# Kernel tuning notes

Measured on AMD Instinct MI355X. Metric: run time of the kernel, lower is better.

The kernel has to match this reference:

```python
import jax, jax.numpy as jnp
import numpy as np

B, N_VIS, N_TXT = 2, 2048, 256
N_HEAD, HEAD_DIM = 16, 64
C = N_HEAD * HEAD_DIM  # 1024
EPS = 1e-6


def setup_inputs() -> dict:
    key = jax.random.key(0)
    ks = jax.random.split(key, 24)
    s = 0.02
    inp = {
        'vis_x': jax.random.normal(ks[0], (B, N_VIS, C), jnp.float32),
        'txt_x': jax.random.normal(ks[1], (B, N_TXT, C), jnp.float32),
        'rope_cos': jax.random.uniform(ks[2], (N_VIS, HEAD_DIM), jnp.float32, -1.0, 1.0),
        'rope_sin': jax.random.uniform(ks[3], (N_VIS, HEAD_DIM), jnp.float32, -1.0, 1.0),
    }
    names = ['vis_qw', 'vis_kw', 'vis_vw', 'vis_ow', 'txt_qw', 'txt_kw', 'txt_vw', 'txt_ow']
    for i, n in enumerate(names):
        inp[n] = jax.random.normal(ks[4 + i], (C, C), jnp.float32) * s
        inp[n[:-1] + 'b'] = jnp.zeros((C,), jnp.float32)
    for n in ['vis_qn', 'vis_kn', 'txt_qn', 'txt_kn']:
        inp[n] = jnp.ones((HEAD_DIM,), jnp.float32)
    return inp


def _heads(x, w, b):
    # x: [B,N,C] -> [B,H,N,D]  (torch Linear: x @ W.T + b)
    y = x @ w.T + b
    Bn, N, _ = y.shape
    return y.reshape(Bn, N, N_HEAD, HEAD_DIM).transpose(0, 2, 1, 3)


def _rmsnorm(x, g):
    return x * jax.lax.rsqrt(jnp.mean(x * x, axis=-1, keepdims=True) + EPS) * g


def _rope(x, cos, sin):
    # interleaved-pair rotation: pairs (x0,x1) -> (-x1, x0)
    xr, xi = x[..., 0::2], x[..., 1::2]
    rot = jnp.stack([-xi, xr], axis=-1).reshape(x.shape)
    return x * cos[None, None] + rot * sin[None, None]


def reference(vis_x, txt_x, rope_cos, rope_sin,
              vis_qw, vis_qb, vis_kw, vis_kb, vis_vw, vis_vb, vis_ow, vis_ob,
              txt_qw, txt_qb, txt_kw, txt_kb, txt_vw, txt_vb, txt_ow, txt_ob,
              vis_qn, vis_kn, txt_qn, txt_kn):
    q_vis = _rmsnorm(_heads(vis_x, vis_qw, vis_qb), vis_qn)
    k_vis = _rmsnorm(_heads(vis_x, vis_kw, vis_kb), vis_kn)
    v_vis = _heads(vis_x, vis_vw, vis_vb)
    q_txt = _rmsnorm(_heads(txt_x, txt_qw, txt_qb), txt_qn)
    k_txt = _rmsnorm(_heads(txt_x, txt_kw, txt_kb), txt_kn)
    v_txt = _heads(txt_x, txt_vw, txt_vb)

    q_vis = _rope(q_vis, rope_cos, rope_sin)
    k_vis = _rope(k_vis, rope_cos, rope_sin)

    q = jnp.concatenate([q_txt, q_vis], axis=2)  # [B,H,S,D]
    k = jnp.concatenate([k_txt, k_vis], axis=2)
    v = jnp.concatenate([v_txt, v_vis], axis=2)

    scale = 1.0 / jnp.sqrt(jnp.asarray(HEAD_DIM, q.dtype))
    scores = jnp.einsum('bhqd,bhkd->bhqk', q, k) * scale
    attn = jax.nn.softmax(scores, axis=-1)
    out = jnp.einsum('bhqk,bhkd->bhqd', attn, v)  # [B,H,S,D]

    txt_out = out[:, :, :N_TXT, :].transpose(0, 2, 1, 3).reshape(q.shape[0], N_TXT, C)
    vis_out = out[:, :, N_TXT:, :].transpose(0, 2, 1, 3).reshape(q.shape[0], N_VIS, C)
    vis_out = vis_out @ vis_ow.T + vis_ob
    txt_out = txt_out @ txt_ow.T + txt_ob
    return (vis_out, txt_out)
```

## Files before the change

### kernel.cpp

```cpp
#include <hip/hip_runtime.h>

typedef _Float16 h8 __attribute__((ext_vector_type(8)));
typedef _Float16 h4 __attribute__((ext_vector_type(4)));
typedef _Float16 h2 __attribute__((ext_vector_type(2)));
typedef float f4 __attribute__((ext_vector_type(4)));
typedef float f16x16 __attribute__((ext_vector_type(16)));

#define LOG2E 1.44269504088896340736f

#define BARRIER_ACQ do { __builtin_amdgcn_s_barrier(); \
                         asm volatile("" ::: "memory"); } while (0)
#define BARRIER_REL do { asm volatile("" ::: "memory"); \
                         __builtin_amdgcn_s_barrier(); } while (0)

__device__ __forceinline__ void gload_lds16(const void* g, void* l) {
    __builtin_amdgcn_global_load_lds(
        (const __attribute__((address_space(1))) void*)g,
        (__attribute__((address_space(3))) void*)l, 16, 0, 0);
}

struct CastArgs { const float* src[10]; _Float16* dst[10]; };

__global__ __launch_bounds__(256) void cast_all_kernel(CastArgs a) {
    int blk = blockIdx.x;
    int seg, rel;
    if (blk < 4096)      { seg = 0; rel = blk; }
    else if (blk < 4608) { seg = 1; rel = blk - 4096; }
    else { int t = blk - 4608; seg = 2 + (t >> 10); rel = t & 1023; }
    long base = ((long)rel * 256 + threadIdx.x) * 4;
    float4 v = *(const float4*)(a.src[seg] + base);
    h4 o = { (_Float16)v.x, (_Float16)v.y, (_Float16)v.z, (_Float16)v.w };
    *(h4*)(a.dst[seg] + base) = o;
}

struct GemmDesc {
    const _Float16* A[2];
    const _Float16* W[2];
    char*           C[2];
    const float*    bias[2][3];
    long bsA[2];
    long aoff[2];
    long bsC[2];
    int  mshift[2];
    int  mcut;
};

template<bool OUT_F32>
__global__ __launch_bounds__(256)
void gemm_kernel(GemmDesc g, int K, int N, int gm, int gn, int xgn)
{
    __shared__ __align__(16) _Float16 As[2][128 * 64];
    __shared__ __align__(16) _Float16 Bs[2][128 * 64];
    const int lane = threadIdx.x & 63;
    const int wave = threadIdx.x >> 6;
    const int lid = blockIdx.x;
    const int xcd = lid & 7;
    const int r0 = lid >> 3;
    const int mtile = (xcd / xgn) * gm + (r0 % gm);
    const int ntile = (xcd % xgn) * gn + (r0 / gm);

    const int seg = mtile >= g.mcut;
    const int mloc = mtile - (seg ? g.mcut : 0);
    const int bidx = mloc >> g.mshift[seg];
    const int min_ = mloc & ((1 << g.mshift[seg]) - 1);
    const _Float16* Ab = g.A[seg] + (long)bidx * g.bsA[seg] + g.aoff[seg]
                         + (long)min_ * 128 * K;
    const _Float16* Bb = g.W[seg] + (long)ntile * 128 * K;
    const long crow0 = (long)bidx * g.bsC[seg] + (long)min_ * 128 * N;

    const int wr = wave >> 1, wc = wave & 1;
    f4 acc[4][4] = {};

    auto stage = [&](int bf, int kt) {
#pragma unroll
        for (int it = 0; it < 4; ++it) {
            int r = wave * 32 + it * 8 + (lane >> 3);
            int lc = (lane & 7) ^ (r & 7);
            gload_lds16((const char*)(Ab + (long)r * K + kt) + lc * 16,
                        (char*)&As[bf][0] + (wave * 32 + it * 8) * 128);
            gload_lds16((const char*)(Bb + (long)r * K + kt) + lc * 16,
                        (char*)&Bs[bf][0] + (wave * 32 + it * 8) * 128);
        }
    };

    const int nk = K >> 6;
    stage(0, 0);
    int buf = 0;
#pragma unroll 1
    for (int ki = 0; ki < nk; ++ki) {
        if (ki + 1 < nk) {
            stage(buf ^ 1, (ki + 1) << 6);
            asm volatile("s_waitcnt vmcnt(8)" ::: "memory");
        } else {
            asm volatile("s_waitcnt vmcnt(0)" ::: "memory");
        }
        BARRIER_ACQ;
#pragma unroll
        for (int kk = 0; kk < 2; ++kk) {
            h8 af[4], bf4[4];
#pragma unroll
            for (int m = 0; m < 4; ++m) {
                int row = wr * 64 + m * 16 + (lane & 15);
                int pc = (kk * 4 + (lane >> 4)) ^ (row & 7);
                af[m] = *(const h8*)(&As[buf][row * 64 + pc * 8]);
            }
#pragma unroll
            for (int n = 0; n < 4; ++n) {
                int row = wc * 64 + n * 16 + (lane & 15);
                int pc = (kk * 4 + (lane >> 4)) ^ (row & 7);
                bf4[n] = *(const h8*)(&Bs[buf][row * 64 + pc * 8]);
            }
#pragma unroll
            for (int m = 0; m < 4; ++m)
#pragma unroll
                for (int n = 0; n < 4; ++n)
                    acc[m][n] = __builtin_amdgcn_mfma_f32_16x16x32_f16(
                        af[m], bf4[n], acc[m][n], 0, 0, 0);
        }
        BARRIER_REL;
        buf ^= 1;
    }

#pragma unroll
    for (int n = 0; n < 4; ++n) {
        int col = ntile * 128 + wc * 64 + n * 16 + (lane & 15);
        const float* bp = (col < 1024) ? g.bias[seg][0]
                        : (col < 2048) ? g.bias[seg][1] : g.bias[seg][2];
        float bv = bp[col & 1023];
#pragma unroll
        for (int m = 0; m < 4; ++m) {
            int lrow = wr * 64 + m * 16 + ((lane >> 4) << 2);
#pragma unroll
            for (int r = 0; r < 4; ++r) {
                float v = acc[m][n][r] + bv;
                long off = crow0 + (long)(lrow + r) * N + col;
                if (OUT_F32) ((float*)g.C[seg])[off] = v;
                else         ((_Float16*)g.C[seg])[off] = (_Float16)v;
            }
        }
    }
}

__device__ __forceinline__ float ssum8(h8 v) {
    float s = 0.f;
#pragma unroll
    for (int j = 0; j < 8; ++j) { float f = (float)v[j]; s += f * f; }
    return s;
}
__device__ __forceinline__ float red8(float s) {
    s += __shfl_xor(s, 1); s += __shfl_xor(s, 2); s += __shfl_xor(s, 4);
    return s;
}
__device__ __forceinline__ h8 norm_rope(h8 v, float rs_, const float* g, float gmul,
                                        const float* cs, const float* sn, int vis) {
    float f[8];
#pragma unroll
    for (int j = 0; j < 8; ++j) f[j] = (float)v[j] * rs_ * g[j] * gmul;
    h8 o;
    if (vis) {
#pragma unroll
        for (int j = 0; j < 8; j += 2) {
            float a = f[j], b = f[j + 1];
            o[j]     = (_Float16)(a * cs[j]     - b * sn[j]);
            o[j + 1] = (_Float16)(b * cs[j + 1] + a * sn[j + 1]);
        }
    } else {
#pragma unroll
        for (int j = 0; j < 8; ++j) o[j] = (_Float16)f[j];
    }
    return o;
}

__global__ __launch_bounds__(256)
void pass2_kernel(const _Float16* __restrict__ Yv, const _Float16* __restrict__ Yt,
                  const float* __restrict__ gqv, const float* __restrict__ gkv_,
                  const float* __restrict__ gqt, const float* __restrict__ gkt,
                  const float* __restrict__ rc, const float* __restrict__ rs,
                  _Float16* __restrict__ Q, _Float16* __restrict__ Kd,
                  _Float16* __restrict__ Vt)
{
    const int wave = threadIdx.x >> 6;
    const int lane = threadIdx.x & 63;
    const int row = blockIdx.x * 4 + wave;
    const int is_vis = row < 4096;
    const _Float16* y;
    const float *gq, *gk;
    int b, n, npos;
    if (is_vis) {
        y = Yv + (long)row * 3072; gq = gqv; gk = gkv_;
        b = row >> 11; n = row & 2047; npos = 256 + n;
    } else {
        int r2 = row - 4096;
        y = Yt + (long)r2 * 3072; gq = gqt; gk = gkt;
        b = r2 >> 8; n = r2 & 255; npos = n;
    }
    const int h0 = lane >> 3;
    const int d0 = (lane & 7) * 8;

    h8 q0 = *(const h8*)(y + lane * 8);
    h8 q1 = *(const h8*)(y + 512 + lane * 8);
    h8 k0 = *(const h8*)(y + 1024 + lane * 8);
    h8 k1 = *(const h8*)(y + 1536 + lane * 8);
    h8 v0 = *(const h8*)(y + 2048 + lane * 8);
    h8 v1 = *(const h8*)(y + 2560 + lane * 8);

    float ga[8], gb[8];
    *(float4*)(ga)     = *(const float4*)(gq + d0);
    *(float4*)(ga + 4) = *(const float4*)(gq + d0 + 4);
    *(float4*)(gb)     = *(const float4*)(gk + d0);
    *(float4*)(gb + 4) = *(const float4*)(gk + d0 + 4);
    float cs[8], sn[8];
    if (is_vis) {
        *(float4*)(cs)     = *(const float4*)(rc + n * 64 + d0);
        *(float4*)(cs + 4) = *(const float4*)(rc + n * 64 + d0 + 4);
        *(float4*)(sn)     = *(const float4*)(rs + n * 64 + d0);
        *(float4*)(sn + 4) = *(const float4*)(rs + n * 64 + d0 + 4);
    }

    const float rq0 = rsqrtf(red8(ssum8(q0)) * (1.0f / 64.0f) + 1e-6f);
    const float rq1 = rsqrtf(red8(ssum8(q1)) * (1.0f / 64.0f) + 1e-6f);
    const float rk0 = rsqrtf(red8(ssum8(k0)) * (1.0f / 64.0f) + 1e-6f);
    const float rk1 = rsqrtf(red8(ssum8(k1)) * (1.0f / 64.0f) + 1e-6f);

    const float qmul = 0.125f * LOG2E;
    const long obA = (((long)b * 16 + h0)      * 2304 + npos) * 64 + d0;
    const long obB = (((long)b * 16 + h0 + 8)  * 2304 + npos) * 64 + d0;
    *(h8*)(Q + obA)  = norm_rope(q0, rq0, ga, qmul, cs, sn, is_vis);
    *(h8*)(Q + obB)  = norm_rope(q1, rq1, ga, qmul, cs, sn, is_vis);
    *(h8*)(Kd + obA) = norm_rope(k0, rk0, gb, 1.0f, cs, sn, is_vis);
    *(h8*)(Kd + obB) = norm_rope(k1, rk1, gb, 1.0f, cs, sn, is_vis);

    const long vbA = ((long)(b * 16 + h0)     * 64 + d0) * 2304 + npos;
    const long vbB = ((long)(b * 16 + h0 + 8) * 64 + d0) * 2304 + npos;
#pragma unroll
    for (int j = 0; j < 8; ++j) {
        Vt[vbA + (long)j * 2304] = v0[j];
        Vt[vbB + (long)j * 2304] = v1[j];
    }
}

__device__ __forceinline__ void attn_stage(const char* Kt, const char* Vt, char* S,
                                           int bufB, int t,
                                           int gK0, int gK1, int gV0, int gV1,
                                           int ldsW) {
    const char* kt = Kt + (long)t * 8192;
    const char* vt = Vt + (long)t * 128;
    gload_lds16(kt + gK0, S + bufB + ldsW);
    gload_lds16(kt + gK1, S + bufB + 4096 + ldsW);
    gload_lds16(vt + gV0, S + 16384 + bufB + ldsW);
    gload_lds16(vt + gV1, S + 16384 + bufB + 4096 + ldsW);
}

__device__ __forceinline__ void pv_half(const float* p, const char* S, int vbase,
                                        const int* off, int kblk,
                                        f16x16* oacc, float& psum) {
    const h2 one2 = {(_Float16)1.f, (_Float16)1.f};
#pragma unroll
    for (int kb = 0; kb < 2; ++kb) {
        unsigned w0 = __builtin_bit_cast(unsigned,
            __builtin_amdgcn_cvt_pkrtz(p[8 * kb + 0], p[8 * kb + 1]));
        unsigned w1 = __builtin_bit_cast(unsigned,
            __builtin_amdgcn_cvt_pkrtz(p[8 * kb + 2], p[8 * kb + 3]));
        unsigned w2 = __builtin_bit_cast(unsigned,
            __builtin_amdgcn_cvt_pkrtz(p[8 * kb + 4], p[8 * kb + 5]));
        unsigned w3 = __builtin_bit_cast(unsigned,
            __builtin_amdgcn_cvt_pkrtz(p[8 * kb + 6], p[8 * kb + 7]));
        psum = __builtin_amdgcn_fdot2(__builtin_bit_cast(h2, w0), one2, psum, false);
        psum = __builtin_amdgcn_fdot2(__builtin_bit_cast(h2, w1), one2, psum, false);
        psum = __builtin_amdgcn_fdot2(__builtin_bit_cast(h2, w2), one2, psum, false);
        psum = __builtin_amdgcn_fdot2(__builtin_bit_cast(h2, w3), one2, psum, false);
        asm("v_permlane32_swap_b32 %0, %1" : "+v"(w0), "+v"(w2));
        asm("v_permlane32_swap_b32 %0, %1" : "+v"(w1), "+v"(w3));
        union { unsigned u[4]; h8 v; } pa;
        pa.u[0] = w0; pa.u[1] = w1; pa.u[2] = w2; pa.u[3] = w3;
#pragma unroll
        for (int dblk = 0; dblk < 2; ++dblk) {
            h8 vb = *(const h8*)(S + vbase + dblk * 4096 + off[kblk * 2 + kb]);
            oacc[dblk] = __builtin_amdgcn_mfma_f32_32x32x16_f16(
                pa.v, vb, oacc[dblk], 0, 0, 0);
        }
    }
}

__device__ __forceinline__ void attn_tile(const char* S, int bufB, const int* off,
                                          const h8* qf, f16x16* oacc, float& psum) {
    const f16x16 kZero = {};
    f16x16 st0, st1;
    {
        h8 ka0 = *(const h8*)(S + bufB + off[0]);
        h8 ka1 = *(const h8*)(S + bufB + 4096 + off[0]);
        st0 = __builtin_amdgcn_mfma_f32_32x32x16_f16(ka0, qf[0], kZero, 0, 0, 0);
        st1 = __builtin_amdgcn_mfma_f32_32x32x16_f16(ka1, qf[0], kZero, 0, 0, 0);
    }
#pragma unroll
    for (int ds = 1; ds < 4; ++ds) {
        h8 ka0 = *(const h8*)(S + bufB + off[ds]);
        h8 ka1 = *(const h8*)(S + bufB + 4096 + off[ds]);
        st0 = __builtin_amdgcn_mfma_f32_32x32x16_f16(ka0, qf[ds], st0, 0, 0, 0);
        st1 = __builtin_amdgcn_mfma_f32_32x32x16_f16(ka1, qf[ds], st1, 0, 0, 0);
    }
    float p0[16], p1[16];
#pragma unroll
    for (int r = 0; r < 16; ++r) { p0[r] = exp2f(st0[r]); p1[r] = exp2f(st1[r]); }
    pv_half(p0, S, 16384 + bufB, off, 0, oacc, psum);
    pv_half(p1, S, 16384 + bufB, off, 1, oacc, psum);
}

__global__ __launch_bounds__(256, 4)
void attn_kernel(const _Float16* __restrict__ Qg,
                 const _Float16* __restrict__ Kg,
                 const _Float16* __restrict__ Vg,
                 _Float16* __restrict__ Op,
                 float* __restrict__ Lp,
                 int nt, int cpx)
{
    __shared__ __align__(16) char S[32768];
    const int lane = threadIdx.x & 63;
    const int wave = threadIdx.x >> 6;
    const int l31 = lane & 31, hi = lane >> 5;
    const int d0 = blockIdx.x;
    const int id = (d0 & 7) * cpx + (d0 >> 3);
    const int split = id / 576;
    const int rem = id - split * 576;
    const int bh = rem / 18;
    const int qb = rem - bh * 18;
    const int b = bh >> 4, h = bh & 15;
    const _Float16* Qbh = Qg + (long)bh * 2304 * 64;
    const char* Kt = (const char*)(Kg + (long)bh * 2304 * 64) + (long)split * nt * 8192;
    const char* Vt = (const char*)(Vg + (long)bh * 64 * 2304) + (long)split * nt * 128;
    _Float16* Ops = Op + (long)split * 4718592;
    float* Lps = Lp + (long)split * 73728;
    const int q0 = qb * 128 + wave * 32;

    h8 qf[4];
#pragma unroll
    for (int ds = 0; ds < 4; ++ds)
        qf[ds] = *(const h8*)(Qbh + (long)(q0 + l31) * 64 + ds * 16 + hi * 8);

    const int sg16 = ((lane & 7) ^ (lane >> 3)) * 16;
    const int rK = wave * 8 + (lane >> 3);
    const int gK0 = rK * 128 + sg16;
    const int gK1 = gK0 + 32 * 128;
    const int gV0 = rK * 4608 + sg16;
    const int gV1 = gV0 + 32 * 4608;
    const int ldsW = wave * 1024;
    int off[4];
#pragma unroll
    for (int j = 0; j < 4; ++j)
        off[j] = l31 * 128 + (((j * 2 + hi) ^ (l31 & 7)) * 16);

    f16x16 oacc[2] = {};
    float psum = 0.f;

    attn_stage(Kt, Vt, S, 0, 0, gK0, gK1, gV0, gV1, ldsW);
    int buf = 0;
#pragma unroll 1
    for (int t = 0; t < nt; ++t) {
        if (t + 1 < nt) {
            attn_stage(Kt, Vt, S, (buf ^ 1) * 8192, t + 1, gK0, gK1, gV0, gV1, ldsW);
            asm volatile("s_waitcnt vmcnt(4)" ::: "memory");
        } else {
            asm volatile("s_waitcnt vmcnt(0)" ::: "memory");
        }
        BARRIER_ACQ;
        __builtin_amdgcn_s_setprio(1);
        attn_tile(S, buf * 8192, off, qf, oacc, psum);
        __builtin_amdgcn_s_setprio(0);
        BARRIER_REL;
        buf ^= 1;
    }

    float lsum = psum + __shfl_xor(psum, 32);
    if (hi == 0) Lps[(long)bh * 2304 + q0 + l31] = lsum;
#pragma unroll
    for (int dblk = 0; dblk < 2; ++dblk) {
        int dcol = h * 64 + dblk * 32 + l31;
#pragma unroll
        for (int r = 0; r < 16; ++r) {
            int qrow = q0 + (r & 3) + 8 * (r >> 2) + 4 * hi;
            Ops[((long)b * 2304 + qrow) * 1024 + dcol] = (_Float16)oacc[dblk][r];
        }
    }
}

__global__ __launch_bounds__(256)
void combine_kernel(const _Float16* __restrict__ Op,
                    const float* __restrict__ Lp,
                    _Float16* __restrict__ Oh, int ns)
{
    long i = ((long)blockIdx.x * 256 + threadIdx.x) * 8;
    long row = i >> 10;
    int bb = row >= 2304;
    int n = (int)row - bb * 2304;
    int h = ((int)i & 1023) >> 6;
    long lidx = ((long)(bb * 16 + h)) * 2304 + n;
    float l = 0.f;
    float acc[8] = {};
    for (int s = 0; s < ns; ++s) {
        l += Lp[(long)s * 73728 + lidx];
        h8 a = *(const h8*)(Op + (long)s * 4718592 + i);
#pragma unroll
        for (int j = 0; j < 8; ++j) acc[j] += (float)a[j];
    }
    float inv = 1.0f / l;
    h8 o;
#pragma unroll
    for (int j = 0; j < 8; ++j) o[j] = (_Float16)(acc[j] * inv);
    *(h8*)(Oh + i) = o;
}

extern "C" void kernel_launch(void* const* d_in, const int* in_sizes, int n_in,
                              void* d_out, int out_size, void* d_ws, size_t ws_size,
                              hipStream_t stream)
{
    const float* vis_x    = (const float*)d_in[0];
    const float* txt_x    = (const float*)d_in[1];
    const float* rope_cos = (const float*)d_in[2];
    const float* rope_sin = (const float*)d_in[3];
    const float* vis_qw = (const float*)d_in[4];
    const float* vis_qb = (const float*)d_in[5];
    const float* vis_kw = (const float*)d_in[6];
    const float* vis_kb = (const float*)d_in[7];
    const float* vis_vw = (const float*)d_in[8];
    const float* vis_vb = (const float*)d_in[9];
    const float* vis_ow = (const float*)d_in[10];
    const float* vis_ob = (const float*)d_in[11];
    const float* txt_qw = (const float*)d_in[12];
    const float* txt_qb = (const float*)d_in[13];
    const float* txt_kw = (const float*)d_in[14];
    const float* txt_kb = (const float*)d_in[15];
    const float* txt_vw = (const float*)d_in[16];
    const float* txt_vb = (const float*)d_in[17];
    const float* txt_ow = (const float*)d_in[18];
    const float* txt_ob = (const float*)d_in[19];
    const float* vis_qn = (const float*)d_in[20];
    const float* vis_kn = (const float*)d_in[21];
    const float* txt_qn = (const float*)d_in[22];
    const float* txt_kn = (const float*)d_in[23];

    char* ws = (char*)d_ws;
    _Float16* Xvis  = (_Float16*)(ws);
    _Float16* Xtxt  = (_Float16*)(ws + 8388608);
    _Float16* Qh    = (_Float16*)(ws);
    _Float16* WqkvV = (_Float16*)(ws + 9437184);
    _Float16* WqkvT = (_Float16*)(ws + 15728640);
    _Float16* WoV   = (_Float16*)(ws + 22020096);
    _Float16* WoT   = (_Float16*)(ws + 24117248);
    _Float16* Yvis  = (_Float16*)(ws + 26214400);
    _Float16* Ytxt  = (_Float16*)(ws + 51380224);
    _Float16* Kh    = (_Float16*)(ws + 54525952);
    _Float16* Vth   = (_Float16*)(ws + 63963136);

    const int ns = (ws_size >= 112328704) ? 4 : 2;
    const int nt = (ns == 4) ? 9 : 18;
    _Float16* OpP;
    if (ns == 4) OpP = (_Float16*)(ws + 73400320);
    else         OpP = (_Float16*)(ws + 26214400);
    float* LpP = (float*)((char*)OpP + (size_t)ns * 9437184);
    _Float16* Oh = OpP;

    CastArgs ca;
    ca.src[0] = vis_x;  ca.dst[0] = Xvis;
    ca.src[1] = txt_x;  ca.dst[1] = Xtxt;
    ca.src[2] = vis_qw; ca.dst[2] = WqkvV;
    ca.src[3] = vis_kw; ca.dst[3] = WqkvV + 1048576;
    ca.src[4] = vis_vw; ca.dst[4] = WqkvV + 2097152;
    ca.src[5] = txt_qw; ca.dst[5] = WqkvT;
    ca.src[6] = txt_kw; ca.dst[6] = WqkvT + 1048576;
    ca.src[7] = txt_vw; ca.dst[7] = WqkvT + 2097152;
    ca.src[8] = vis_ow; ca.dst[8] = WoV;
    ca.src[9] = txt_ow; ca.dst[9] = WoT;
    cast_all_kernel<<<12800, 256, 0, stream>>>(ca);

    GemmDesc gq;
    gq.A[0] = Xvis;  gq.A[1] = Xtxt;
    gq.W[0] = WqkvV; gq.W[1] = WqkvT;
    gq.C[0] = (char*)Yvis; gq.C[1] = (char*)Ytxt;
    gq.bias[0][0] = vis_qb; gq.bias[0][1] = vis_kb; gq.bias[0][2] = vis_vb;
    gq.bias[1][0] = txt_qb; gq.bias[1][1] = txt_kb; gq.bias[1][2] = txt_vb;
    gq.bsA[0] = 0; gq.bsA[1] = 0;
    gq.aoff[0] = 0; gq.aoff[1] = 0;
    gq.bsC[0] = 0; gq.bsC[1] = 0;
    gq.mshift[0] = 5; gq.mshift[1] = 5;
    gq.mcut = 32;
    gemm_kernel<false><<<864, 256, 0, stream>>>(gq, 1024, 3072, 9, 12, 2);

    pass2_kernel<<<1152, 256, 0, stream>>>(
        Yvis, Ytxt, vis_qn, vis_kn, txt_qn, txt_kn, rope_cos, rope_sin,
        Qh, Kh, Vth);

    attn_kernel<<<576 * ns, 256, 0, stream>>>(Qh, Kh, Vth, OpP, LpP, nt, 72 * ns);
    combine_kernel<<<2304, 256, 0, stream>>>(OpP, LpP, Oh, ns);

    GemmDesc go;
    go.A[0] = Oh; go.A[1] = Oh;
    go.W[0] = WoV; go.W[1] = WoT;
    go.C[0] = (char*)d_out; go.C[1] = (char*)((float*)d_out + 4194304);
    go.bias[0][0] = vis_ob; go.bias[0][1] = vis_ob; go.bias[0][2] = vis_ob;
    go.bias[1][0] = txt_ob; go.bias[1][1] = txt_ob; go.bias[1][2] = txt_ob;
    go.bsA[0] = 2359296;  go.bsA[1] = 2359296;
    go.aoff[0] = 262144;  go.aoff[1] = 0;
    go.bsC[0] = 2097152;  go.bsC[1] = 262144;
    go.mshift[0] = 4; go.mshift[1] = 1;
    go.mcut = 32;
    gemm_kernel<true><<<288, 256, 0, stream>>>(go, 1024, 1024, 9, 4, 2);
}
```

Before: 192.7 us.

## Halve attention KV tile to raise occupancy; add LDS-staged V transpose kernel

Moves the V transpose out of pass2, which used scattered 2-byte strided stores, into a dedicated kernel that stages 128-row tiles through shared memory and writes coalesced 16-byte rows. The attention kernel now processes 32-key tiles instead of 64, halving LDS to 16KB and raising the launch bound to 8 blocks per SM. The loop trip count doubles to cover the same keys. This trades more barriers and loop iterations, plus an extra kernel launch, for higher occupancy and cheaper V layout writes.

```diff
diff --git a/kernel.cpp b/kernel.cpp
--- a/kernel.cpp
+++ b/kernel.cpp
@@ -176,8 +176,7 @@
                   const float* __restrict__ gqv, const float* __restrict__ gkv_,
                   const float* __restrict__ gqt, const float* __restrict__ gkt,
                   const float* __restrict__ rc, const float* __restrict__ rs,
-                  _Float16* __restrict__ Q, _Float16* __restrict__ Kd,
-                  _Float16* __restrict__ Vt)
+                  _Float16* __restrict__ Q, _Float16* __restrict__ Kd)
 {
     const int wave = threadIdx.x >> 6;
     const int lane = threadIdx.x & 63;
@@ -201,8 +200,6 @@
     h8 q1 = *(const h8*)(y + 512 + lane * 8);
     h8 k0 = *(const h8*)(y + 1024 + lane * 8);
     h8 k1 = *(const h8*)(y + 1536 + lane * 8);
-    h8 v0 = *(const h8*)(y + 2048 + lane * 8);
-    h8 v1 = *(const h8*)(y + 2560 + lane * 8);
 
     float ga[8], gb[8];
     *(float4*)(ga)     = *(const float4*)(gq + d0);
@@ -229,32 +226,64 @@
     *(h8*)(Q + obB)  = norm_rope(q1, rq1, ga, qmul, cs, sn, is_vis);
     *(h8*)(Kd + obA) = norm_rope(k0, rk0, gb, 1.0f, cs, sn, is_vis);
     *(h8*)(Kd + obB) = norm_rope(k1, rk1, gb, 1.0f, cs, sn, is_vis);
-
-    const long vbA = ((long)(b * 16 + h0)     * 64 + d0) * 2304 + npos;
-    const long vbB = ((long)(b * 16 + h0 + 8) * 64 + d0) * 2304 + npos;
-#pragma unroll
-    for (int j = 0; j < 8; ++j) {
-        Vt[vbA + (long)j * 2304] = v0[j];
-        Vt[vbB + (long)j * 2304] = v1[j];
-    }
-}
-
-__device__ __forceinline__ void attn_stage(const char* Kt, const char* Vt, char* S,
-                                           int bufB, int t,
-                                           int gK0, int gK1, int gV0, int gV1,
-                                           int ldsW) {
-    const char* kt = Kt + (long)t * 8192;
-    const char* vt = Vt + (long)t * 128;
-    gload_lds16(kt + gK0, S + bufB + ldsW);
-    gload_lds16(kt + gK1, S + bufB + 4096 + ldsW);
-    gload_lds16(vt + gV0, S + 16384 + bufB + ldsW);
-    gload_lds16(vt + gV1, S + 16384 + bufB + 4096 + ldsW);
-}
-
-__device__ __forceinline__ void pv_half(const float* p, const char* S, int vbase,
-                                        const int* off, int kblk,
-                                        f16x16* oacc, float& psum) {
+}
+
+__global__ __launch_bounds__(256)
+void vtrans_kernel(const _Float16* __restrict__ Yv, const _Float16* __restrict__ Yt,
+                   _Float16* __restrict__ Vt)
+{
+    __shared__ _Float16 T[64 * 136];
+    const int blk = blockIdx.x;
+    const int bh = blk / 18, ntl = blk - bh * 18;
+    const int b = bh >> 4, h = bh & 15;
+    const int npos0 = ntl * 128;
+    const _Float16* Y; long m0;
+    if (ntl >= 2) { Y = Yv; m0 = (long)b * 2048 + (npos0 - 256); }
+    else          { Y = Yt; m0 = (long)b * 256 + npos0; }
+    const int t = threadIdx.x;
+    const _Float16* src = Y + m0 * 3072 + 2048 + h * 64;
+#pragma unroll
+    for (int ri = 0; ri < 4; ++ri) {
+        int row = ri * 32 + (t >> 3);
+        int c8 = t & 7;
+        h8 v = *(const h8*)(src + (long)row * 3072 + c8 * 8);
+#pragma unroll
+        for (int j = 0; j < 8; ++j)
+            T[(c8 * 8 + j) * 136 + row] = v[j];
+    }
+    __syncthreads();
+    const int d = t >> 2, ch = t & 3;
+    _Float16* dst = Vt + ((long)bh * 64 + d) * 2304 + npos0 + ch * 32;
+#pragma unroll
+    for (int k = 0; k < 4; ++k)
+        *(h8*)(dst + k * 8) = *(const h8*)(&T[d * 136 + ch * 32 + k * 8]);
+}
+
+__device__ __forceinline__ void attn_stage32(const char* Kt, const char* Vt, char* S,
+                                             int bufB, int t,
+                                             int gK, int gV, int ldsW) {
+    gload_lds16(Kt + (long)t * 4096 + gK, S + bufB + ldsW);
+    gload_lds16(Vt + (long)t * 64 + gV, S + 8192 + bufB + ldsW);
+}
+
+__device__ __forceinline__ void attn_tile32(const char* S, int bufB,
+                                            const int* offK, const int* offV,
+                                            const h8* qf, f16x16* oacc, float& psum) {
+    const f16x16 kZero = {};
     const h2 one2 = {(_Float16)1.f, (_Float16)1.f};
+    f16x16 st;
+    {
+        h8 ka = *(const h8*)(S + bufB + offK[0]);
+        st = __builtin_amdgcn_mfma_f32_32x32x16_f16(ka, qf[0], kZero, 0, 0, 0);
+    }
+#pragma unroll
+    for (int ds = 1; ds < 4; ++ds) {
+        h8 ka = *(const h8*)(S + bufB + offK[ds]);
+        st = __builtin_amdgcn_mfma_f32_32x32x16_f16(ka, qf[ds], st, 0, 0, 0);
+    }
+    float p[16];
+#pragma unroll
+    for (int r = 0; r < 16; ++r) p[r] = exp2f(st[r]);
 #pragma unroll
     for (int kb = 0; kb < 2; ++kb) {
         unsigned w0 = __builtin_bit_cast(unsigned,
@@ -275,38 +304,14 @@
         pa.u[0] = w0; pa.u[1] = w1; pa.u[2] = w2; pa.u[3] = w3;
 #pragma unroll
         for (int dblk = 0; dblk < 2; ++dblk) {
-            h8 vb = *(const h8*)(S + vbase + dblk * 4096 + off[kblk * 2 + kb]);
+            h8 vb = *(const h8*)(S + 8192 + bufB + dblk * 2048 + offV[kb]);
             oacc[dblk] = __builtin_amdgcn_mfma_f32_32x32x16_f16(
                 pa.v, vb, oacc[dblk], 0, 0, 0);
         }
     }
 }
 
-__device__ __forceinline__ void attn_tile(const char* S, int bufB, const int* off,
-                                          const h8* qf, f16x16* oacc, float& psum) {
-    const f16x16 kZero = {};
-    f16x16 st0, st1;
-    {
-        h8 ka0 = *(const h8*)(S + bufB + off[0]);
-        h8 ka1 = *(const h8*)(S + bufB + 4096 + off[0]);
-        st0 = __builtin_amdgcn_mfma_f32_32x32x16_f16(ka0, qf[0], kZero, 0, 0, 0);
-        st1 = __builtin_amdgcn_mfma_f32_32x32x16_f16(ka1, qf[0], kZero, 0, 0, 0);
-    }
-#pragma unroll
-    for (int ds = 1; ds < 4; ++ds) {
-        h8 ka0 = *(const h8*)(S + bufB + off[ds]);
-        h8 ka1 = *(const h8*)(S + bufB + 4096 + off[ds]);
-        st0 = __builtin_amdgcn_mfma_f32_32x32x16_f16(ka0, qf[ds], st0, 0, 0, 0);
-        st1 = __builtin_amdgcn_mfma_f32_32x32x16_f16(ka1, qf[ds], st1, 0, 0, 0);
-    }
-    float p0[16], p1[16];
-#pragma unroll
-    for (int r = 0; r < 16; ++r) { p0[r] = exp2f(st0[r]); p1[r] = exp2f(st1[r]); }
-    pv_half(p0, S, 16384 + bufB, off, 0, oacc, psum);
-    pv_half(p1, S, 16384 + bufB, off, 1, oacc, psum);
-}
-
-__global__ __launch_bounds__(256, 4)
+__global__ __launch_bounds__(256, 8)
 void attn_kernel(const _Float16* __restrict__ Qg,
                  const _Float16* __restrict__ Kg,
                  const _Float16* __restrict__ Vg,
@@ -314,7 +319,7 @@
                  float* __restrict__ Lp,
                  int nt, int cpx)
 {
-    __shared__ __align__(16) char S[32768];
+    __shared__ __align__(16) char S[16384];
     const int lane = threadIdx.x & 63;
     const int wave = threadIdx.x >> 6;
     const int l31 = lane & 31, hi = lane >> 5;
@@ -326,8 +331,8 @@
     const int qb = rem - bh * 18;
     const int b = bh >> 4, h = bh & 15;
     const _Float16* Qbh = Qg + (long)bh * 2304 * 64;
-    const char* Kt = (const char*)(Kg + (long)bh * 2304 * 64) + (long)split * nt * 8192;
-    const char* Vt = (const char*)(Vg + (long)bh * 64 * 2304) + (long)split * nt * 128;
+    const char* Kt = (const char*)(Kg + (long)bh * 2304 * 64) + (long)split * nt * 4096;
+    const char* Vt = (const char*)(Vg + (long)bh * 64 * 2304) + (long)split * nt * 64;
     _Float16* Ops = Op + (long)split * 4718592;
     float* Lps = Lp + (long)split * 73728;
     const int q0 = qb * 128 + wave * 32;
@@ -337,34 +342,35 @@
     for (int ds = 0; ds < 4; ++ds)
         qf[ds] = *(const h8*)(Qbh + (long)(q0 + l31) * 64 + ds * 16 + hi * 8);
 
-    const int sg16 = ((lane & 7) ^ (lane >> 3)) * 16;
     const int rK = wave * 8 + (lane >> 3);
-    const int gK0 = rK * 128 + sg16;
-    const int gK1 = gK0 + 32 * 128;
-    const int gV0 = rK * 4608 + sg16;
-    const int gV1 = gV0 + 32 * 4608;
+    const int gK = rK * 128 + (((lane & 7) ^ (rK & 7)) * 16);
+    const int rV = wave * 16 + (lane >> 2);
+    const int gV = rV * 4608 + (((lane & 3) ^ (rV & 3)) * 16);
     const int ldsW = wave * 1024;
-    int off[4];
+    int offK[4], offV[2];
 #pragma unroll
     for (int j = 0; j < 4; ++j)
-        off[j] = l31 * 128 + (((j * 2 + hi) ^ (l31 & 7)) * 16);
+        offK[j] = l31 * 128 + (((j * 2 + hi) ^ (l31 & 7)) * 16);
+#pragma unroll
+    for (int j = 0; j < 2; ++j)
+        offV[j] = l31 * 64 + (((j * 2 + hi) ^ (l31 & 3)) * 16);
 
     f16x16 oacc[2] = {};
     float psum = 0.f;
 
-    attn_stage(Kt, Vt, S, 0, 0, gK0, gK1, gV0, gV1, ldsW);
+    attn_stage32(Kt, Vt, S, 0, 0, gK, gV, ldsW);
     int buf = 0;
 #pragma unroll 1
     for (int t = 0; t < nt; ++t) {
         if (t + 1 < nt) {
-            attn_stage(Kt, Vt, S, (buf ^ 1) * 8192, t + 1, gK0, gK1, gV0, gV1, ldsW);
-            asm volatile("s_waitcnt vmcnt(4)" ::: "memory");
+            attn_stage32(Kt, Vt, S, (buf ^ 1) * 4096, t + 1, gK, gV, ldsW);
+            asm volatile("s_waitcnt vmcnt(2)" ::: "memory");
         } else {
             asm volatile("s_waitcnt vmcnt(0)" ::: "memory");
         }
         BARRIER_ACQ;
         __builtin_amdgcn_s_setprio(1);
-        attn_tile(S, buf * 8192, off, qf, oacc, psum);
+        attn_tile32(S, buf * 4096, offK, offV, qf, oacc, psum);
         __builtin_amdgcn_s_setprio(0);
         BARRIER_REL;
         buf ^= 1;
@@ -452,7 +458,7 @@
     _Float16* Vth   = (_Float16*)(ws + 63963136);
 
     const int ns = (ws_size >= 112328704) ? 4 : 2;
-    const int nt = (ns == 4) ? 9 : 18;
+    const int nt = (ns == 4) ? 18 : 36;
     _Float16* OpP;
     if (ns == 4) OpP = (_Float16*)(ws + 73400320);
     else         OpP = (_Float16*)(ws + 26214400);
@@ -486,8 +492,8 @@
     gemm_kernel<false><<<864, 256, 0, stream>>>(gq, 1024, 3072, 9, 12, 2);
 
     pass2_kernel<<<1152, 256, 0, stream>>>(
-        Yvis, Ytxt, vis_qn, vis_kn, txt_qn, txt_kn, rope_cos, rope_sin,
-        Qh, Kh, Vth);
+        Yvis, Ytxt, vis_qn, vis_kn, txt_qn, txt_kn, rope_cos, rope_sin, Qh, Kh);
+    vtrans_kernel<<<576, 256, 0, stream>>>(Yvis, Ytxt, Vth);
 
     attn_kernel<<<576 * ns, 256, 0, stream>>>(Qh, Kh, Vth, OpP, LpP, nt, 72 * ns);
     combine_kernel<<<2304, 256, 0, stream>>>(OpP, LpP, Oh, ns);
```

After: 310.7 us. +61.2%, slower.
